# Kernel tuning notes

Hardware: AMD Instinct MI355X
Metric: run time of the kernel (lower is better)

## Reference

```python
import jax, jax.numpy as jnp
import numpy as np

B, A, F, D, C = 256, 128, 512, 6, 512  # batch, max_atoms, atom_features, max_degree, conv_width


def setup_inputs() -> dict:
    key = jax.random.key(0)
    k1, k2, k3, k4 = jax.random.split(key, 4)
    atoms = jax.random.normal(k1, (B, A, F), dtype=jnp.float32)
    # neighbour indices in [0, A); pad entries beyond each atom's degree with -1
    neigh = jax.random.randint(k2, (B, A, D), 0, A)
    deg = jax.random.randint(k3, (B, A, 1), 0, D)  # degrees in 0..D-1
    bonds = jnp.where(jnp.arange(D)[None, None, :] < deg, neigh, -1)
    # one Dense(conv_width) per degree: stacked kernels [D, F, C] and biases [D, C]
    W = jax.random.normal(k4, (D, F, C), dtype=jnp.float32) * 0.02
    b = jnp.zeros((D, C), dtype=jnp.float32)
    return {"atoms": atoms, "bonds": bonds, "W": W, "b": b}


def reference(atoms, bonds, W, b):
    d_max = bonds.shape[-1]
    # per-atom degree = count of non -1 neighbour slots  [B, A, 1]
    degrees = jnp.sum(bonds != -1, axis=-1, keepdims=True)
    # shift lookup by 1 so that padded (-1) neighbours index a zero row
    padded = jnp.pad(atoms, ((0, 0), (1, 1), (0, 0)))  # [B, A+2, F]
    idx = bonds + 1  # [B, A, D]
    # per-sample gather of neighbour features -> [B, A, D, F]
    neigh_feats = jax.vmap(lambda ref, i: ref[i])(padded, idx)
    summed = jnp.sum(neigh_feats, axis=2) + atoms  # [B, A, F]
    # apply all degree-specific dense layers, then mask-select by degree
    dense = jnp.einsum('baf,dfc->badc', summed, W) + b  # [B, A, D, C]
    masks = (degrees[..., None] == jnp.arange(d_max).reshape(1, 1, d_max, 1)).astype(dense.dtype)
    return jnp.sum(dense * masks, axis=2)  # [B, A, C]
```

## Files before the change

### kernel.cpp

```cpp
#include <hip/hip_runtime.h>
#include <hip/hip_bf16.h>


#define NB 256
#define NA 128
#define NF 512
#define ND 6
#define NC 512
#define NATOMS (NB * NA)

typedef __attribute__((ext_vector_type(8))) short frag8;
typedef __attribute__((ext_vector_type(4))) float f32x4;

static __device__ inline unsigned short f2bu(float f) {
    __hip_bfloat16 h = __float2bfloat16(f);
    return *reinterpret_cast<unsigned short*>(&h);
}
static __device__ inline unsigned int pack2(float a, float b) {
    return (unsigned int)f2bu(a) | ((unsigned int)f2bu(b) << 16);
}
static __device__ inline void async16(const void* g, void* l) {
    __builtin_amdgcn_global_load_lds(
        (const __attribute__((address_space(1))) void*)g,
        (__attribute__((address_space(3))) void*)l, 16, 0, 0);
}

__global__ void transpose_w(const float* __restrict__ W,
                            __hip_bfloat16* __restrict__ Wt,
                            int* __restrict__ counts) {
    if (blockIdx.x == 0 && blockIdx.y == 0 && blockIdx.z == 0 &&
        threadIdx.y == 0 && threadIdx.x < ND)
        counts[threadIdx.x] = 0;
    __shared__ float t[32][33];
    const int d  = blockIdx.z;
    const int c0 = blockIdx.x * 32;
    const int f0 = blockIdx.y * 32;
    #pragma unroll
    for (int r = 0; r < 32; r += 8)
        t[threadIdx.y + r][threadIdx.x] =
            W[((size_t)(d * NF + f0 + threadIdx.y + r)) * NC + c0 + threadIdx.x];
    __syncthreads();
    #pragma unroll
    for (int r = 0; r < 32; r += 8)
        Wt[((size_t)(d * NC + c0 + threadIdx.y + r)) * NF + f0 + threadIdx.x] =
            __float2bfloat16(t[threadIdx.x][threadIdx.y + r]);
}

__global__ __launch_bounds__(256) void bucket_atoms(
    const int* __restrict__ bonds, int* __restrict__ counts,
    int* __restrict__ bucket) {
    __shared__ int lcnt[ND];
    __shared__ int lbase[ND];
    const int tid = threadIdx.x;
    if (tid < ND) lcnt[tid] = 0;
    __syncthreads();
    int deg[4], loc[4], gg[4];
    #pragma unroll
    for (int i = 0; i < 4; ++i) {
        int g = blockIdx.x * 1024 + i * 256 + tid;
        gg[i] = g;
        int dg = 0;
        #pragma unroll
        for (int j = 0; j < ND; ++j) dg += (bonds[g * ND + j] >= 0);
        deg[i] = dg;
        loc[i] = atomicAdd(&lcnt[dg], 1);
    }
    __syncthreads();
    if (tid < ND) lbase[tid] = atomicAdd(&counts[tid], lcnt[tid]);
    __syncthreads();
    #pragma unroll
    for (int i = 0; i < 4; ++i)
        bucket[deg[i] * NATOMS + lbase[deg[i]] + loc[i]] = gg[i];
}

__global__ __launch_bounds__(256) void sum_neigh(
    const float* __restrict__ atoms, const int* __restrict__ bonds,
    __hip_bfloat16* __restrict__ summed) {
    const int tid  = threadIdx.x;
    const int wave = tid >> 6;
    const int lane = tid & 63;
    const int swz  = (blockIdx.x & 7) * (NATOMS / 4 / 8) + (blockIdx.x >> 3);
    const int g    = swz * 4 + wave;
    const float4* a4 = (const float4*)atoms;

    int   nb[ND];
    float msk[ND];
    #pragma unroll
    for (int j = 0; j < ND; ++j) {
        int n = bonds[g * ND + j];
        msk[j] = (n >= 0) ? 1.0f : 0.0f;
        nb[j]  = (n >= 0) ? n : 0;
    }
    const int rowbase = g & ~(NA - 1);

    float4 s0 = a4[(size_t)g * 128 + lane];
    float4 s1 = a4[(size_t)g * 128 + 64 + lane];
    float4 v0[ND], v1[ND];
    #pragma unroll
    for (int j = 0; j < ND; ++j) {
        const size_t base = (size_t)(rowbase + nb[j]) * 128;
        v0[j] = a4[base + lane];
        v1[j] = a4[base + 64 + lane];
    }
    #pragma unroll
    for (int j = 0; j < ND; ++j) {
        s0.x = fmaf(v0[j].x, msk[j], s0.x); s0.y = fmaf(v0[j].y, msk[j], s0.y);
        s0.z = fmaf(v0[j].z, msk[j], s0.z); s0.w = fmaf(v0[j].w, msk[j], s0.w);
        s1.x = fmaf(v1[j].x, msk[j], s1.x); s1.y = fmaf(v1[j].y, msk[j], s1.y);
        s1.z = fmaf(v1[j].z, msk[j], s1.z); s1.w = fmaf(v1[j].w, msk[j], s1.w);
    }

    uint2 o0, o1;
    o0.x = pack2(s0.x, s0.y); o0.y = pack2(s0.z, s0.w);
    o1.x = pack2(s1.x, s1.y); o1.y = pack2(s1.z, s1.w);
    ((uint2*)summed)[(size_t)g * 128 + lane] = o0;
    ((uint2*)summed)[(size_t)g * 128 + 64 + lane] = o1;
}

__global__ __launch_bounds__(256, 2) void gemm_deg(
    const __hip_bfloat16* __restrict__ summed, const __hip_bfloat16* __restrict__ Wt,
    const float* __restrict__ bias, const int* __restrict__ counts,
    const int* __restrict__ bucket, float* __restrict__ out) {
    const int L  = blockIdx.x + 24 * blockIdx.y;
    const int q  = L >> 3;
    const int p  = ((q >> 2) << 3) + (L & 7);
    const int d  = p % ND;
    const int m0 = (p / ND) * 128;
    const int n0 = (q & 3) * 128;
    const int Md = counts[d];
    if (m0 >= Md) return;

    __shared__ __align__(16) __hip_bfloat16 sA[2][128 * 64];
    __shared__ __align__(16) __hip_bfloat16 sB[2][128 * 64];
    __shared__ int sRows[128];

    const int tid = threadIdx.x;
    if (tid < 128) {
        int r = m0 + tid;
        sRows[tid] = (r < Md) ? bucket[d * NATOMS + r] : -1;
    }
    __syncthreads();

    const int lane = tid & 63;
    const int w    = tid >> 6;
    const int srow = lane >> 3;
    const int seg  = lane & 7;

    const char* smB = (const char*)summed;
    const char* wtB = (const char*)Wt + (size_t)(d * NC + n0) * (NF * 2);
    size_t gA[4];
    int    rowc[4];
    #pragma unroll
    for (int c = 0; c < 4; ++c) {
        rowc[c] = w * 32 + c * 8 + srow;
        int qr = sRows[rowc[c]];
        gA[c] = (size_t)((qr < 0) ? 0 : qr) * (NF * 2);
    }

    const int quad = lane >> 4, l16 = lane & 15;
    const int wy = w >> 1, wx = w & 1;

    f32x4 acc[4][4];
    #pragma unroll
    for (int i = 0; i < 4; ++i)
        #pragma unroll
        for (int j = 0; j < 4; ++j) acc[i][j] = (f32x4)0.0f;

    auto stage = [&](int buf, int kt) {
        const int koff = kt * 128 + seg * 16;
        #pragma unroll
        for (int c = 0; c < 4; ++c) {
            async16(smB + gA[c] + koff, &sA[buf][(w * 32 + c * 8) * 64]);
            async16(wtB + (size_t)rowc[c] * (NF * 2) + koff, &sB[buf][(w * 32 + c * 8) * 64]);
        }
    };
    auto compute = [&](int buf) {
        #pragma unroll
        for (int ks = 0; ks < 64; ks += 32) {
            frag8 aF[4], bF[4];
            #pragma unroll
            for (int i = 0; i < 4; ++i)
                aF[i] = *(const frag8*)&sA[buf][(wy * 64 + i * 16 + l16) * 64 + ks + quad * 8];
            #pragma unroll
            for (int j = 0; j < 4; ++j)
                bF[j] = *(const frag8*)&sB[buf][(wx * 64 + j * 16 + l16) * 64 + ks + quad * 8];
            #pragma unroll
            for (int i = 0; i < 4; ++i)
                #pragma unroll
                for (int j = 0; j < 4; ++j)
                    acc[i][j] = __builtin_amdgcn_mfma_f32_16x16x32_bf16(
                        aF[i], bF[j], acc[i][j], 0, 0, 0);
        }
    };

    stage(0, 0);
    __syncthreads();
    int cur = 0;
    #pragma unroll
    for (int kt = 1; kt < NF / 64; ++kt) {
        stage(cur ^ 1, kt);
        compute(cur);
        __syncthreads();
        cur ^= 1;
    }
    compute(cur);

    #pragma unroll
    for (int j = 0; j < 4; ++j) {
        const int n = n0 + wx * 64 + j * 16 + l16;
        const float bv = bias[d * NC + n];
        #pragma unroll
        for (int i = 0; i < 4; ++i) {
            #pragma unroll
            for (int r = 0; r < 4; ++r) {
                const int tr = wy * 64 + i * 16 + quad * 4 + r;
                const int g  = sRows[tr];
                if (g >= 0)
                    out[(size_t)g * NC + n] = acc[i][j][r] + bv;
            }
        }
    }
}

extern "C" void kernel_launch(void* const* d_in, const int* in_sizes, int n_in,
                              void* d_out, int out_size, void* d_ws, size_t ws_size,
                              hipStream_t stream) {
    const float* atoms = (const float*)d_in[0];
    const int*   bonds = (const int*)d_in[1];
    const float* W     = (const float*)d_in[2];
    const float* bias  = (const float*)d_in[3];
    float* out = (float*)d_out;

    char* ws = (char*)d_ws;
    int* counts = (int*)ws;
    int* bucket = (int*)(ws + 1024);
    __hip_bfloat16* Wt     = (__hip_bfloat16*)(ws + 1024 + 786432);
    __hip_bfloat16* summed = (__hip_bfloat16*)(ws + 1024 + 786432 + 3145728);

    transpose_w<<<dim3(NC / 32, NF / 32, ND), dim3(32, 8), 0, stream>>>(W, Wt, counts);

    bucket_atoms<<<NATOMS / 1024, 256, 0, stream>>>(bonds, counts, bucket);

    sum_neigh<<<NATOMS / 4, 256, 0, stream>>>(atoms, bonds, summed);

    gemm_deg<<<dim3(24, NATOMS / 128), 256, 0, stream>>>(
        summed, Wt, bias, counts, bucket, out);
}
```

Before: 199.1 us.

## Fuse prep kernels and triple-buffer GEMM with swizzled LDS and smaller K tiles

```diff
diff --git a/kernel.cpp b/kernel.cpp
--- a/kernel.cpp
+++ b/kernel.cpp
@@ -9,6 +9,10 @@
 #define NC 512
 #define NATOMS (NB * NA)
 
+#define NT_TRANS 1536
+#define NT_BUCK  32
+#define NT_SUM   8192
+
 typedef __attribute__((ext_vector_type(8))) short frag8;
 typedef __attribute__((ext_vector_type(4))) float f32x4;
 
@@ -25,61 +29,60 @@
         (__attribute__((address_space(3))) void*)l, 16, 0, 0);
 }
 
-__global__ void transpose_w(const float* __restrict__ W,
-                            __hip_bfloat16* __restrict__ Wt,
-                            int* __restrict__ counts) {
-    if (blockIdx.x == 0 && blockIdx.y == 0 && blockIdx.z == 0 &&
-        threadIdx.y == 0 && threadIdx.x < ND)
-        counts[threadIdx.x] = 0;
+__global__ __launch_bounds__(256) void prep(
+    const float* __restrict__ W, __hip_bfloat16* __restrict__ Wt,
+    const int* __restrict__ bonds, int* __restrict__ counts,
+    int* __restrict__ bucket,
+    const float* __restrict__ atoms, __hip_bfloat16* __restrict__ summed) {
+    const int bid = blockIdx.x;
+    const int tid = threadIdx.x;
     __shared__ float t[32][33];
-    const int d  = blockIdx.z;
-    const int c0 = blockIdx.x * 32;
-    const int f0 = blockIdx.y * 32;
-    #pragma unroll
-    for (int r = 0; r < 32; r += 8)
-        t[threadIdx.y + r][threadIdx.x] =
-            W[((size_t)(d * NF + f0 + threadIdx.y + r)) * NC + c0 + threadIdx.x];
-    __syncthreads();
-    #pragma unroll
-    for (int r = 0; r < 32; r += 8)
-        Wt[((size_t)(d * NC + c0 + threadIdx.y + r)) * NF + f0 + threadIdx.x] =
-            __float2bfloat16(t[threadIdx.x][threadIdx.y + r]);
-}
-
-__global__ __launch_bounds__(256) void bucket_atoms(
-    const int* __restrict__ bonds, int* __restrict__ counts,
-    int* __restrict__ bucket) {
     __shared__ int lcnt[ND];
     __shared__ int lbase[ND];
-    const int tid = threadIdx.x;
-    if (tid < ND) lcnt[tid] = 0;
-    __syncthreads();
-    int deg[4], loc[4], gg[4];
-    #pragma unroll
-    for (int i = 0; i < 4; ++i) {
-        int g = blockIdx.x * 1024 + i * 256 + tid;
-        gg[i] = g;
-        int dg = 0;
-        #pragma unroll
-        for (int j = 0; j < ND; ++j) dg += (bonds[g * ND + j] >= 0);
-        deg[i] = dg;
-        loc[i] = atomicAdd(&lcnt[dg], 1);
-    }
-    __syncthreads();
-    if (tid < ND) lbase[tid] = atomicAdd(&counts[tid], lcnt[tid]);
-    __syncthreads();
-    #pragma unroll
-    for (int i = 0; i < 4; ++i)
-        bucket[deg[i] * NATOMS + lbase[deg[i]] + loc[i]] = gg[i];
-}
-
-__global__ __launch_bounds__(256) void sum_neigh(
-    const float* __restrict__ atoms, const int* __restrict__ bonds,
-    __hip_bfloat16* __restrict__ summed) {
-    const int tid  = threadIdx.x;
+
+    if (bid < NT_TRANS) {
+        const int tx = tid & 31, ty = tid >> 5;
+        const int c0 = (bid & 15) * 32;
+        const int f0 = ((bid >> 4) & 15) * 32;
+        const int d  = bid >> 8;
+        #pragma unroll
+        for (int r = 0; r < 32; r += 8)
+            t[ty + r][tx] =
+                W[((size_t)(d * NF + f0 + ty + r)) * NC + c0 + tx];
+        __syncthreads();
+        #pragma unroll
+        for (int r = 0; r < 32; r += 8)
+            Wt[((size_t)(d * NC + c0 + ty + r)) * NF + f0 + tx] =
+                __float2bfloat16(t[tx][ty + r]);
+        return;
+    }
+    if (bid < NT_TRANS + NT_BUCK) {
+        const int b = bid - NT_TRANS;
+        if (tid < ND) lcnt[tid] = 0;
+        __syncthreads();
+        int deg[4], loc[4], gg[4];
+        #pragma unroll
+        for (int i = 0; i < 4; ++i) {
+            int g = b * 1024 + i * 256 + tid;
+            gg[i] = g;
+            int dg = 0;
+            #pragma unroll
+            for (int j = 0; j < ND; ++j) dg += (bonds[g * ND + j] >= 0);
+            deg[i] = dg;
+            loc[i] = atomicAdd(&lcnt[dg], 1);
+        }
+        __syncthreads();
+        if (tid < ND) lbase[tid] = atomicAdd(&counts[tid], lcnt[tid]);
+        __syncthreads();
+        #pragma unroll
+        for (int i = 0; i < 4; ++i)
+            bucket[deg[i] * NATOMS + lbase[deg[i]] + loc[i]] = gg[i];
+        return;
+    }
+    const int sbid = bid - (NT_TRANS + NT_BUCK);
     const int wave = tid >> 6;
     const int lane = tid & 63;
-    const int swz  = (blockIdx.x & 7) * (NATOMS / 4 / 8) + (blockIdx.x >> 3);
+    const int swz  = (sbid & 7) * (NT_SUM / 8) + (sbid >> 3);
     const int g    = swz * 4 + wave;
     const float4* a4 = (const float4*)atoms;
 
@@ -117,7 +120,7 @@
     ((uint2*)summed)[(size_t)g * 128 + 64 + lane] = o1;
 }
 
-__global__ __launch_bounds__(256, 2) void gemm_deg(
+__global__ __launch_bounds__(256, 3) void gemm_deg(
     const __hip_bfloat16* __restrict__ summed, const __hip_bfloat16* __restrict__ Wt,
     const float* __restrict__ bias, const int* __restrict__ counts,
     const int* __restrict__ bucket, float* __restrict__ out) {
@@ -130,8 +133,8 @@
     const int Md = counts[d];
     if (m0 >= Md) return;
 
-    __shared__ __align__(16) __hip_bfloat16 sA[2][128 * 64];
-    __shared__ __align__(16) __hip_bfloat16 sB[2][128 * 64];
+    __shared__ __align__(16) __hip_bfloat16 sA[3][128 * 32];
+    __shared__ __align__(16) __hip_bfloat16 sB[3][128 * 32];
     __shared__ int sRows[128];
 
     const int tid = threadIdx.x;
@@ -143,21 +146,22 @@
 
     const int lane = tid & 63;
     const int w    = tid >> 6;
-    const int srow = lane >> 3;
-    const int seg  = lane & 7;
+
+    const int srow2 = tid >> 2;
+    const int slot  = tid & 3;
+    const int gs    = slot ^ ((srow2 >> 1) & 3);
 
     const char* smB = (const char*)summed;
     const char* wtB = (const char*)Wt + (size_t)(d * NC + n0) * (NF * 2);
-    size_t gA[4];
-    int    rowc[4];
-    #pragma unroll
-    for (int c = 0; c < 4; ++c) {
-        rowc[c] = w * 32 + c * 8 + srow;
-        int qr = sRows[rowc[c]];
+    size_t gA[2];
+    #pragma unroll
+    for (int c = 0; c < 2; ++c) {
+        int qr = sRows[c * 64 + srow2];
         gA[c] = (size_t)((qr < 0) ? 0 : qr) * (NF * 2);
     }
 
     const int quad = lane >> 4, l16 = lane & 15;
+    const int xr2  = (l16 >> 1) & 3;
     const int wy = w >> 1, wx = w & 1;
 
     f32x4 acc[4][4];
@@ -167,43 +171,47 @@
         for (int j = 0; j < 4; ++j) acc[i][j] = (f32x4)0.0f;
 
     auto stage = [&](int buf, int kt) {
-        const int koff = kt * 128 + seg * 16;
-        #pragma unroll
-        for (int c = 0; c < 4; ++c) {
-            async16(smB + gA[c] + koff, &sA[buf][(w * 32 + c * 8) * 64]);
-            async16(wtB + (size_t)rowc[c] * (NF * 2) + koff, &sB[buf][(w * 32 + c * 8) * 64]);
+        const int koff = kt * 64 + gs * 16;
+        #pragma unroll
+        for (int c = 0; c < 2; ++c) {
+            async16(smB + gA[c] + koff, &sA[buf][c * 2048 + w * 512]);
+            async16(wtB + (size_t)(c * 64 + srow2) * (NF * 2) + koff,
+                    &sB[buf][c * 2048 + w * 512]);
         }
     };
     auto compute = [&](int buf) {
-        #pragma unroll
-        for (int ks = 0; ks < 64; ks += 32) {
-            frag8 aF[4], bF[4];
-            #pragma unroll
-            for (int i = 0; i < 4; ++i)
-                aF[i] = *(const frag8*)&sA[buf][(wy * 64 + i * 16 + l16) * 64 + ks + quad * 8];
+        frag8 aF[4], bF[4];
+        #pragma unroll
+        for (int i = 0; i < 4; ++i)
+            aF[i] = *(const frag8*)&sA[buf][(wy * 64 + i * 16 + l16) * 32 +
+                                            ((quad ^ xr2) << 3)];
+        #pragma unroll
+        for (int j = 0; j < 4; ++j)
+            bF[j] = *(const frag8*)&sB[buf][(wx * 64 + j * 16 + l16) * 32 +
+                                            ((quad ^ xr2) << 3)];
+        #pragma unroll
+        for (int i = 0; i < 4; ++i)
             #pragma unroll
             for (int j = 0; j < 4; ++j)
-                bF[j] = *(const frag8*)&sB[buf][(wx * 64 + j * 16 + l16) * 64 + ks + quad * 8];
-            #pragma unroll
-            for (int i = 0; i < 4; ++i)
-                #pragma unroll
-                for (int j = 0; j < 4; ++j)
-                    acc[i][j] = __builtin_amdgcn_mfma_f32_16x16x32_bf16(
-                        aF[i], bF[j], acc[i][j], 0, 0, 0);
-        }
+                acc[i][j] = __builtin_amdgcn_mfma_f32_16x16x32_bf16(
+                    aF[i], bF[j], acc[i][j], 0, 0, 0);
     };
 
     stage(0, 0);
-    __syncthreads();
-    int cur = 0;
-    #pragma unroll
-    for (int kt = 1; kt < NF / 64; ++kt) {
-        stage(cur ^ 1, kt);
-        compute(cur);
-        __syncthreads();
-        cur ^= 1;
-    }
-    compute(cur);
+    stage(1, 1);
+    #pragma unroll
+    for (int kt = 0; kt < NF / 32; ++kt) {
+        if (kt < NF / 32 - 1)
+            asm volatile("s_waitcnt vmcnt(4)" ::: "memory");
+        else
+            asm volatile("s_waitcnt vmcnt(0)" ::: "memory");
+        __builtin_amdgcn_sched_barrier(0);
+        __builtin_amdgcn_s_barrier();
+        if (kt + 2 < NF / 32) stage((kt + 2) % 3, kt + 2);
+        __builtin_amdgcn_s_setprio(1);
+        compute(kt % 3);
+        __builtin_amdgcn_s_setprio(0);
+    }
 
     #pragma unroll
     for (int j = 0; j < 4; ++j) {
@@ -237,11 +245,10 @@
     __hip_bfloat16* Wt     = (__hip_bfloat16*)(ws + 1024 + 786432);
     __hip_bfloat16* summed = (__hip_bfloat16*)(ws + 1024 + 786432 + 3145728);
 
-    transpose_w<<<dim3(NC / 32, NF / 32, ND), dim3(32, 8), 0, stream>>>(W, Wt, counts);
-
-    bucket_atoms<<<NATOMS / 1024, 256, 0, stream>>>(bonds, counts, bucket);
-
-    sum_neigh<<<NATOMS / 4, 256, 0, stream>>>(atoms, bonds, summed);
+    hipMemsetAsync(counts, 0, 1024, stream);
+
+    prep<<<NT_TRANS + NT_BUCK + NT_SUM, 256, 0, stream>>>(
+        W, Wt, bonds, counts, bucket, atoms, summed);
 
     gemm_deg<<<dim3(24, NATOMS / 128), 256, 0, stream>>>(
         summed, Wt, bias, counts, bucket, out);
```

Measured after the change: 176.8 us. -11.2%, faster.
